# Performance work log

Hardware: AMD Instinct MI355X
Metric: run time of the kernel (lower is better)

## Reference

```python
import jax, jax.numpy as jnp
from jax import lax
import numpy as np

B, N, K = 8, 4096, 64          # clouds, points per cloud, max neighbors
N1, N2 = N // 2, N // 8        # fps ratio 0.5, then 0.25
R1, R2 = 0.2, 0.4              # ball-query radii


def setup_inputs() -> dict:
    key = jax.random.key(0)
    ks = jax.random.split(key, 7)
    def w(k, i, o):
        return jax.random.normal(k, (i, o), jnp.float32) / np.sqrt(i).astype(np.float32)
    return {
        "pos": jax.random.uniform(ks[0], (B, N, 3), jnp.float32),
        "w1a": w(ks[1], 3, 64),    "b1a": jnp.zeros(64, jnp.float32),
        "w1b": w(ks[2], 64, 64),   "b1b": jnp.zeros(64, jnp.float32),
        "w2a": w(ks[3], 67, 128),  "b2a": jnp.zeros(128, jnp.float32),
        "w2b": w(ks[4], 128, 128), "b2b": jnp.zeros(128, jnp.float32),
        "w3a": w(ks[5], 131, 256), "b3a": jnp.zeros(256, jnp.float32),
        "w3b": w(ks[6], 256, 1024),"b3b": jnp.zeros(1024, jnp.float32),
    }


def fps(pos, n_samples):
    # farthest point sampling, deterministic start at index 0. pos: [n, 3]
    d0 = jnp.sum((pos - pos[0]) ** 2, axis=-1)
    def step(mind, _):
        nxt = jnp.argmax(mind)
        d = jnp.sum((pos - pos[nxt]) ** 2, axis=-1)
        return jnp.minimum(mind, d), nxt
    _, idxs = lax.scan(step, d0, None, length=n_samples - 1)
    return jnp.concatenate([jnp.zeros((1,), idxs.dtype), idxs])


def ball_query(centers, pts, r):
    # up to K neighbors within radius r (nearest-first); centers are a subset of pts
    d2 = jnp.sum((centers[:, None, :] - pts[None, :, :]) ** 2, axis=-1)  # [M, n]
    neg = jnp.where(d2 <= r * r, -d2, -jnp.inf)
    vals, nbr = lax.top_k(neg, K)
    return nbr, vals > -jnp.inf  # [M, K] indices, validity mask


def mlp(x, w1, b1, w2, b2, relu_last):
    h = jax.nn.relu(x @ w1 + b1) @ w2 + b2
    return jax.nn.relu(h) if relu_last else h


def masked_max(h, mask):
    # max over neighbor axis; every center has itself as a valid neighbor
    return jnp.max(jnp.where(mask[..., None], h, -jnp.inf), axis=1)


def reference(pos, w1a, b1a, w1b, b1b, w2a, b2a, w2b, b2b, w3a, b3a, w3b, b3b):
    def single(p):  # p: [N, 3]
        # SA1: x is None -> per-edge input is relative position only
        idx1 = fps(p, N1)
        c1 = p[idx1]                                   # [N1, 3]
        nbr1, m1 = ball_query(c1, p, R1)               # [N1, K]
        rel1 = p[nbr1] - c1[:, None, :]                # [N1, K, 3]
        x1 = masked_max(mlp(rel1, w1a, b1a, w1b, b1b, True), m1)   # [N1, 64]
        # SA2: per-edge input is [x_j, pos_j - pos_i]
        idx2 = fps(c1, N2)
        c2 = c1[idx2]                                  # [N2, 3]
        nbr2, m2 = ball_query(c2, c1, R2)              # [N2, K]
        feat2 = jnp.concatenate([x1[nbr2], c1[nbr2] - c2[:, None, :]], axis=-1)  # [N2,K,67]
        x2 = masked_max(mlp(feat2, w2a, b2a, w2b, b2b, True), m2)  # [N2, 128]
        # Global SA: MLP on [x, pos] then global max pool
        g = mlp(jnp.concatenate([x2, c2], axis=-1), w3a, b3a, w3b, b3b, False)   # [N2,1024]
        return jnp.max(g, axis=0)                      # [1024]
    return jax.vmap(single)(pos)                       # [B, 1024]
```

## Files before the change

### kernel.cpp

```cpp
#include <hip/hip_runtime.h>
#include <cstdint>
#include <cstddef>


static constexpr int Bc = 8;
static constexpr int Np = 4096;
static constexpr int Kn = 64;
static constexpr int M1 = 2048;
static constexpr int M2 = 512;
static constexpr int LDX = 132;

#define DEVINL __device__ __forceinline__

DEVINL float d2_exact(float ax, float ay, float az, float bx, float by, float bz) {
    float dx = __fsub_rn(ax, bx);
    float dy = __fsub_rn(ay, by);
    float dz = __fsub_rn(az, bz);
    float xx = __fmul_rn(dx, dx);
    float yy = __fmul_rn(dy, dy);
    float zz = __fmul_rn(dz, dz);
    return __fadd_rn(__fadd_rn(xx, yy), zz);
}

template <int CTRL, int RM, int BM>
DEVINL unsigned long long dpp_max_step(unsigned long long k) {
    unsigned lo = (unsigned)k, hi = (unsigned)(k >> 32);
    unsigned slo = (unsigned)__builtin_amdgcn_update_dpp(0, (int)lo, CTRL, RM, BM, true);
    unsigned shi = (unsigned)__builtin_amdgcn_update_dpp(0, (int)hi, CTRL, RM, BM, true);
    unsigned long long s = ((unsigned long long)shi << 32) | (unsigned long long)slo;
    return s > k ? s : k;
}

DEVINL unsigned long long wave_max_u64_dpp(unsigned long long k) {
    k = dpp_max_step<0x111, 0xf, 0xf>(k);
    k = dpp_max_step<0x112, 0xf, 0xf>(k);
    k = dpp_max_step<0x114, 0xf, 0xf>(k);
    k = dpp_max_step<0x118, 0xf, 0xf>(k);
    k = dpp_max_step<0x142, 0xa, 0xf>(k);
    k = dpp_max_step<0x143, 0xc, 0xf>(k);
    return k;
}

DEVINL unsigned mort3(unsigned v) {
    return (v & 1u) | ((v & 2u) << 2) | ((v & 4u) << 4);
}

DEVINL unsigned cell_of(float x, float y, float z) {
    int ix = (int)(x * 8.0f); ix = ix < 0 ? 0 : (ix > 7 ? 7 : ix);
    int iy = (int)(y * 8.0f); iy = iy < 0 ? 0 : (iy > 7 ? 7 : iy);
    int iz = (int)(z * 8.0f); iz = iz < 0 ? 0 : (iz > 7 ? 7 : iz);
    return mort3((unsigned)ix) | (mort3((unsigned)iy) << 1) | (mort3((unsigned)iz) << 2);
}

DEVINL unsigned* scan512(unsigned* h0, unsigned* h1, int t) {
    unsigned* src = h0; unsigned* dst = h1;
    for (int d = 1; d < 512; d <<= 1) {
        unsigned v = src[t];
        if (t >= d) v += src[t - d];
        dst[t] = v;
        __syncthreads();
        unsigned* tmp = src; src = dst; dst = tmp;
    }
    return src;
}

template <int NPTS, int PT>
DEVINL void fps_chunk_body(const float* __restrict__ srcpts,
                           float4* __restrict__ scp_g,
                           float* __restrict__ mind_g,
                           char* smem, int t, int lane,
                           int s_begin, int s_end) {
    constexpr int NT = NPTS / PT;
    float4* scp = (float4*)smem;
    unsigned* h0 = (unsigned*)(smem + 65536);
    unsigned* h1 = (unsigned*)(smem + 67584);
    unsigned long long* slots = (unsigned long long*)(smem + 69632);
    float* journal = (float*)(smem + 69664);

    float px[PT], py[PT], pz[PT], mind[PT];
    unsigned oi[PT];
    unsigned long long ck = 0;

    if (s_begin == 0) {
        float gx[PT], gy[PT], gz[PT];
        unsigned gc[PT];
        #pragma unroll
        for (int j = 0; j < PT; ++j) {
            int p = j * NT + t;
            gx[j] = srcpts[p * 3 + 0];
            gy[j] = srcpts[p * 3 + 1];
            gz[j] = srcpts[p * 3 + 2];
            gc[j] = cell_of(gx[j], gy[j], gz[j]);
        }
        float x0 = srcpts[0], y0 = srcpts[1], z0 = srcpts[2];
        h0[t] = 0;
        if (t == 0) { slots[0] = 0; slots[1] = 0; slots[2] = 0; }
        __syncthreads();
        #pragma unroll
        for (int j = 0; j < PT; ++j) atomicAdd(&h0[gc[j]], 1u);
        __syncthreads();
        unsigned cnt = h0[t];
        unsigned* inc = scan512(h0, h1, t);
        inc[t] -= cnt;
        __syncthreads();
        #pragma unroll
        for (int j = 0; j < PT; ++j) {
            unsigned p = atomicAdd(&inc[gc[j]], 1u);
            unsigned key = ((0xFFFu - (unsigned)(j * NT + t)) << 12) | p;
            scp[p] = make_float4(gx[j], gy[j], gz[j], __uint_as_float(key));
        }
        __syncthreads();
        for (int k = t; k < NPTS; k += NT) scp_g[k] = scp[k];
        #pragma unroll
        for (int j = 0; j < PT; ++j) {
            float4 v = scp[t * PT + j];
            px[j] = v.x; py[j] = v.y; pz[j] = v.z;
            oi[j] = __float_as_uint(v.w);
        }
        #pragma unroll
        for (int j = 0; j < PT; ++j) {
            float d = d2_exact(px[j], py[j], pz[j], x0, y0, z0);
            mind[j] = d;
            unsigned long long kj =
                ((unsigned long long)__float_as_uint(d) << 24) | (unsigned long long)oi[j];
            if (kj > ck) ck = kj;
        }
        if (t == 0) { journal[0] = x0; journal[1] = y0; journal[2] = z0; }
    } else {
        if (t == 0) { slots[0] = 0; slots[1] = 0; slots[2] = 0; }
        for (int k = t; k < NPTS; k += NT) scp[k] = scp_g[k];
        __syncthreads();
        #pragma unroll
        for (int j = 0; j < PT; ++j) {
            float4 v = scp[t * PT + j];
            px[j] = v.x; py[j] = v.y; pz[j] = v.z;
            oi[j] = __float_as_uint(v.w);
        }
        #pragma unroll
        for (int j = 0; j < PT; ++j) mind[j] = mind_g[t * PT + j];
        #pragma unroll
        for (int j = 0; j < PT; ++j) {
            unsigned long long kj =
                ((unsigned long long)__float_as_uint(mind[j]) << 24) |
                (unsigned long long)oi[j];
            if (kj > ck) ck = kj;
        }
    }

    float lox = px[0], hix = px[0], loy = py[0], hiy = py[0], loz = pz[0], hiz = pz[0];
    #pragma unroll
    for (int j = 1; j < PT; ++j) {
        lox = fminf(lox, px[j]); hix = fmaxf(hix, px[j]);
        loy = fminf(loy, py[j]); hiy = fmaxf(hiy, py[j]);
        loz = fminf(loz, pz[j]); hiz = fmaxf(hiz, pz[j]);
    }

    float bmax = __uint_as_float((unsigned)(ck >> 24));
    unsigned long long wkey = wave_max_u64_dpp(ck);
    if (lane == 63) atomicMax(&slots[1], wkey);

    int rd = 1, wr = 2, rs = 0;
    for (int s = (s_begin == 0 ? 1 : s_begin); s < s_end; ++s) {
        __syncthreads();
        unsigned long long km = slots[rd];
        if (t == 0) slots[rs] = 0;
        unsigned spos = (unsigned)km & 0xFFFu;
        float4 cc = scp[spos];
        float cx = cc.x, cy = cc.y, cz = cc.z;
        if (t == 0) {
            int jj = (s - s_begin) * 3;
            journal[jj + 0] = cx; journal[jj + 1] = cy; journal[jj + 2] = cz;
        }
        float dxv = fmaxf(fmaxf(lox - cx, cx - hix), 0.0f);
        float dyv = fmaxf(fmaxf(loy - cy, cy - hiy), 0.0f);
        float dzv = fmaxf(fmaxf(loz - cz, cz - hiz), 0.0f);
        float L = dxv * dxv + dyv * dyv + dzv * dzv;
        bool fire = (L * 0.999f <= bmax);
        if (fire) {
            unsigned long long nck = 0;
            #pragma unroll
            for (int j = 0; j < PT; ++j) {
                float d = d2_exact(px[j], py[j], pz[j], cx, cy, cz);
                float m = fminf(mind[j], d);
                mind[j] = m;
                unsigned long long kj =
                    ((unsigned long long)__float_as_uint(m) << 24) | (unsigned long long)oi[j];
                if (kj > nck) nck = kj;
            }
            ck = nck;
            bmax = __uint_as_float((unsigned)(ck >> 24));
        }
        if (__ballot(fire) != 0ull) wkey = wave_max_u64_dpp(ck);
        if (lane == 63) atomicMax(&slots[wr], wkey);
        int nrd = wr; wr = rs; rs = rd; rd = nrd;
    }
    __syncthreads();
    #pragma unroll
    for (int j = 0; j < PT; ++j) mind_g[t * PT + j] = mind[j];
}

template <int NPT>
DEVINL void bq_core(const float* __restrict__ pb, float cx, float cy, float cz,
                    float r2, int* out, uint2* buf, int lane) {
    constexpr int CH = NPT / 64;
    constexpr int CAP = 1024;
    const unsigned r2b = __float_as_uint(r2);
    const unsigned long long lml = (1ull << lane) - 1ull;

    int cnt = 0;
    #pragma unroll 8
    for (int j = 0; j < CH; ++j) {
        int p = j * 64 + lane;
        float d = d2_exact(pb[p * 3 + 0], pb[p * 3 + 1], pb[p * 3 + 2], cx, cy, cz);
        cnt += __popcll(__ballot(__float_as_uint(d) <= r2b));
    }

    if (cnt <= Kn) {
        int basep = 0;
        #pragma unroll 8
        for (int j = 0; j < CH; ++j) {
            int p = j * 64 + lane;
            float d = d2_exact(pb[p * 3 + 0], pb[p * 3 + 1], pb[p * 3 + 2], cx, cy, cz);
            bool v = __float_as_uint(d) <= r2b;
            unsigned long long mk = __ballot(v);
            if (v) out[basep + __popcll(mk & lml)] = p;
            basep += __popcll(mk);
        }
        if (lane >= cnt) out[lane] = -1;
    } else if (cnt <= CAP) {
        int basep = 0;
        #pragma unroll 8
        for (int j = 0; j < CH; ++j) {
            int p = j * 64 + lane;
            float d = d2_exact(pb[p * 3 + 0], pb[p * 3 + 1], pb[p * 3 + 2], cx, cy, cz);
            unsigned ubj = __float_as_uint(d);
            bool v = ubj <= r2b;
            unsigned long long mk = __ballot(v);
            if (v) buf[basep + __popcll(mk & lml)] = make_uint2(ubj, (unsigned)p);
            basep += __popcll(mk);
        }
        const int C2 = (cnt + 63) >> 6;
        unsigned cb[CAP / 64], ci[CAP / 64];
        #pragma unroll
        for (int e = 0; e < CAP / 64; ++e) {
            if (e >= C2) break;
            int p = e * 64 + lane;
            uint2 v = buf[p];
            cb[e] = (p < cnt) ? v.x : 0xFFFFFFFFu;
            ci[e] = v.y;
        }
        unsigned lo = 0, hi = r2b;
        while (lo < hi) {
            unsigned mid = lo + ((hi - lo) >> 1);
            int c = 0;
            #pragma unroll
            for (int e = 0; e < CAP / 64; ++e) {
                if (e >= C2) break;
                c += __popcll(__ballot(cb[e] <= mid));
            }
            if (c >= Kn) hi = mid; else lo = mid + 1;
        }
        const unsigned tt = lo;
        int cntLess = 0;
        #pragma unroll
        for (int e = 0; e < CAP / 64; ++e) {
            if (e >= C2) break;
            cntLess += __popcll(__ballot(cb[e] < tt));
        }
        const int quota = Kn - cntLess;
        int baseLt = 0, eqseen = 0;
        #pragma unroll
        for (int e = 0; e < CAP / 64; ++e) {
            if (e >= C2) break;
            bool lt = cb[e] < tt;
            bool eq = cb[e] == tt;
            unsigned long long mlt = __ballot(lt);
            unsigned long long meq = __ballot(eq);
            if (lt) out[baseLt + __popcll(mlt & lml)] = (int)ci[e];
            if (eq) {
                int rr = eqseen + __popcll(meq & lml);
                if (rr < quota) out[cntLess + rr] = (int)ci[e];
            }
            baseLt += __popcll(mlt);
            eqseen += __popcll(meq);
        }
    } else {
        unsigned lo = 0, hi = r2b;
        while (lo < hi) {
            unsigned mid = lo + ((hi - lo) >> 1);
            int c = 0;
            for (int j = 0; j < CH; ++j) {
                int p = j * 64 + lane;
                float d = d2_exact(pb[p * 3 + 0], pb[p * 3 + 1], pb[p * 3 + 2], cx, cy, cz);
                c += __popcll(__ballot(__float_as_uint(d) <= mid));
            }
            if (c >= Kn) hi = mid; else lo = mid + 1;
        }
        const unsigned tt = lo;
        int cntLess = 0;
        for (int j = 0; j < CH; ++j) {
            int p = j * 64 + lane;
            float d = d2_exact(pb[p * 3 + 0], pb[p * 3 + 1], pb[p * 3 + 2], cx, cy, cz);
            cntLess += __popcll(__ballot(__float_as_uint(d) < tt));
        }
        const int quota = Kn - cntLess;
        int baseLt = 0, eqseen = 0;
        for (int j = 0; j < CH; ++j) {
            int p = j * 64 + lane;
            float d = d2_exact(pb[p * 3 + 0], pb[p * 3 + 1], pb[p * 3 + 2], cx, cy, cz);
            unsigned ubj = __float_as_uint(d);
            bool lt = ubj < tt;
            bool eq = ubj == tt;
            unsigned long long mlt = __ballot(lt);
            unsigned long long meq = __ballot(eq);
            if (lt) out[baseLt + __popcll(mlt & lml)] = p;
            if (eq) {
                int rr = eqseen + __popcll(meq & lml);
                if (rr < quota) out[cntLess + rr] = p;
            }
            baseLt += __popcll(mlt);
            eqseen += __popcll(meq);
        }
    }
}

DEVINL void mlp1_core(const float* __restrict__ pb, float cx, float cy, float cz,
                      const int* nbrL, const float* __restrict__ w1aT,
                      const float* __restrict__ w1bT, const float* __restrict__ b1b,
                      float* __restrict__ orow, int lane) {
    const int ii = nbrL[lane];
    const bool valid = ii >= 0;
    const int i2 = valid ? ii : 0;
    const float* pp = pb + (size_t)i2 * 3;
    float rx = pp[0] - cx, ry = pp[1] - cy, rz = pp[2] - cz;
    float h1[64];
    #pragma unroll
    for (int h = 0; h < 64; ++h) {
        float4 wv = ((const float4*)w1aT)[h];
        float a = fmaf(rx, wv.x, fmaf(ry, wv.y, fmaf(rz, wv.z, wv.w)));
        h1[h] = fmaxf(a, 0.0f);
    }
    for (int c4 = 0; c4 < 16; ++c4) {
        float v4[4];
        #pragma unroll
        for (int cq = 0; cq < 4; ++cq) {
            int c = c4 * 4 + cq;
            float acc = b1b[c];
            const float4* wr = (const float4*)(w1bT + (size_t)c * 64);
            #pragma unroll
            for (int q = 0; q < 16; ++q) {
                float4 wv = wr[q];
                acc = fmaf(h1[4 * q + 0], wv.x, acc);
                acc = fmaf(h1[4 * q + 1], wv.y, acc);
                acc = fmaf(h1[4 * q + 2], wv.z, acc);
                acc = fmaf(h1[4 * q + 3], wv.w, acc);
            }
            float v = fmaxf(acc, 0.0f);
            v = valid ? v : -__builtin_inff();
            #pragma unroll
            for (int o = 32; o > 0; o >>= 1) v = fmaxf(v, __shfl_xor(v, o, 64));
            v4[cq] = v;
        }
        if (lane == 0)
            ((float4*)orow)[c4] = make_float4(v4[0], v4[1], v4[2], v4[3]);
    }
}

DEVINL void mlp2_core(const float* __restrict__ x1b, const float* __restrict__ c1b,
                      float cx, float cy, float cz, const int* nbrL,
                      const float* __restrict__ w2aT, const float* __restrict__ w2bT,
                      const float* __restrict__ b2b, float* __restrict__ orow,
                      int lane) {
    const int ii = nbrL[lane];
    const bool valid = ii >= 0;
    const int i2 = valid ? ii : 0;

    float x[68];
    const float4* xr = (const float4*)(x1b + (size_t)i2 * 64);
    #pragma unroll
    for (int q = 0; q < 16; ++q) {
        float4 v = xr[q];
        x[4 * q + 0] = v.x; x[4 * q + 1] = v.y;
        x[4 * q + 2] = v.z; x[4 * q + 3] = v.w;
    }
    const float* cp = c1b + (size_t)i2 * 3;
    x[64] = cp[0] - cx;
    x[65] = cp[1] - cy;
    x[66] = cp[2] - cz;
    x[67] = 0.0f;

    float h1[128];
    #pragma unroll
    for (int h = 0; h < 128; ++h) {
        const float4* r4 = (const float4*)(w2aT + (size_t)h * 80);
        float acc = 0.0f;
        #pragma unroll
        for (int q = 0; q < 16; ++q) {
            float4 wv = r4[q];
            acc = fmaf(x[4 * q + 0], wv.x, acc);
            acc = fmaf(x[4 * q + 1], wv.y, acc);
            acc = fmaf(x[4 * q + 2], wv.z, acc);
            acc = fmaf(x[4 * q + 3], wv.w, acc);
        }
        float4 tl = r4[16];
        acc = fmaf(x[64], tl.x, acc);
        acc = fmaf(x[65], tl.y, acc);
        acc = fmaf(x[66], tl.z, acc);
        acc += tl.w;
        h1[h] = fmaxf(acc, 0.0f);
    }
    for (int c4 = 0; c4 < 32; ++c4) {
        float v4[4];
        #pragma unroll
        for (int cq = 0; cq < 4; ++cq) {
            int c = c4 * 4 + cq;
            float acc = b2b[c];
            const float4* wr = (const float4*)(w2bT + (size_t)c * 128);
            #pragma unroll
            for (int q = 0; q < 32; ++q) {
                float4 wv = wr[q];
                acc = fmaf(h1[4 * q + 0], wv.x, acc);
                acc = fmaf(h1[4 * q + 1], wv.y, acc);
                acc = fmaf(h1[4 * q + 2], wv.z, acc);
                acc = fmaf(h1[4 * q + 3], wv.w, acc);
            }
            float v = fmaxf(acc, 0.0f);
            v = valid ? v : -__builtin_inff();
            #pragma unroll
            for (int o = 32; o > 0; o >>= 1) v = fmaxf(v, __shfl_xor(v, o, 64));
            v4[cq] = v;
        }
        if (lane == 0) {
            orow[c4 * 4 + 0] = v4[0]; orow[c4 * 4 + 1] = v4[1];
            orow[c4 * 4 + 2] = v4[2]; orow[c4 * 4 + 3] = v4[3];
        }
    }
}

__global__ __launch_bounds__(512)
__attribute__((amdgpu_waves_per_eu(2, 2)))
void stage_kernel(int fps_stage, int s_begin, int s_end,
                  int w_stage, int w_begin, int wsh,
                  const float* __restrict__ pos, float* __restrict__ c1,
                  float* __restrict__ c2, float* __restrict__ X,
                  float* __restrict__ x1,
                  float4* __restrict__ scp1_g, float* __restrict__ mind1_g,
                  float4* __restrict__ scp2_g, float* __restrict__ mind2_g,
                  const float* __restrict__ w1a, const float* __restrict__ b1a,
                  const float* __restrict__ w1b, const float* __restrict__ w2a,
                  const float* __restrict__ b2a, const float* __restrict__ w2b,
                  float* __restrict__ w1aT, float* __restrict__ w1bT,
                  float* __restrict__ w2aT, float* __restrict__ w2bT,
                  const float* __restrict__ b1b, const float* __restrict__ b2b) {
    __shared__ __align__(16) char smem[94720];
    const int t = threadIdx.x;
    const int lane = t & 63;
    const int wid = t >> 6;

    if (fps_stage > 0 && blockIdx.x < Bc) {
        const int b = blockIdx.x;
        float* journal = (float*)(smem + 69664);
        if (fps_stage == 1) {
            fps_chunk_body<Np, 8>(pos + (size_t)b * Np * 3, scp1_g + (size_t)b * Np,
                                  mind1_g + (size_t)b * Np, smem, t, lane,
                                  s_begin, s_end);
            int n = (s_end - s_begin) * 3;
            for (int i = t; i < n; i += 512)
                c1[(size_t)b * M1 * 3 + s_begin * 3 + i] = journal[i];
        } else {
            fps_chunk_body<M1, 4>(c1 + (size_t)b * M1 * 3, scp2_g + (size_t)b * M1,
                                  mind2_g + (size_t)b * M1, smem, t, lane,
                                  s_begin, s_end);
            int n = (s_end - s_begin) * 3;
            for (int i = t; i < n; i += 512)
                c2[(size_t)b * M2 * 3 + s_begin * 3 + i] = journal[i];
            for (int i = t; i < n; i += 512) {
                int s = i / 3, k = i - s * 3;
                X[(size_t)(b * M2 + s_begin + s) * LDX + 128 + k] = journal[i];
            }
        }
        return;
    }

    const int wb = (fps_stage > 0) ? (int)blockIdx.x - Bc : (int)blockIdx.x;
    const int nw = (fps_stage > 0) ? (int)gridDim.x - Bc : (int)gridDim.x;

    if (w_stage == 1) {
        int i = wb * 512 + t;
        if (i < 64 * 4) {
            int h = i >> 2, d = i & 3;
            w1aT[i] = (d < 3) ? w1a[d * 64 + h] : b1a[h];
        }
        if (i < 64 * 64) {
            int c = i >> 6, h = i & 63;
            w1bT[i] = w1b[h * 64 + c];
        }
        if (i < 128 * 80) {
            int h = i / 80, d = i - h * 80;
            w2aT[i] = (d < 67) ? w2a[d * 128 + h] : ((d == 67) ? b2a[h] : 0.0f);
        }
        if (i < 128 * 128) {
            int c = i >> 7, h = i & 127;
            w2bT[i] = w2b[h * 128 + c];
        }
        return;
    }

    if (w_stage == 2) {
        uint2* cbuf = (uint2*)smem + (size_t)wid * 1024;
        int* nbrL = (int*)(smem + 65536) + wid * 64;
        const int span_mask = (1 << wsh) - 1;
        const int ntasks = Bc << wsh;
        for (int task = wb * 8 + wid; task < ntasks; task += nw * 8) {
            const int b = task >> wsh;
            const int s = w_begin + (task & span_mask);
            const int w = b * M1 + s;
            const float* cr = c1 + (size_t)w * 3;
            float cx = cr[0], cy = cr[1], cz = cr[2];
            const float* pb = pos + (size_t)b * Np * 3;
            bq_core<Np>(pb, cx, cy, cz, (float)(0.2 * 0.2), nbrL, cbuf, lane);
            mlp1_core(pb, cx, cy, cz, nbrL, w1aT, w1bT, b1b,
                      x1 + (size_t)w * 64, lane);
        }
        return;
    }

    if (w_stage == 3) {
        uint2* cbuf = (uint2*)smem + (size_t)wid * 1024;
        int* nbrL = (int*)(smem + 65536) + wid * 64;
        const int span_mask = (1 << wsh) - 1;
        const int ntasks = Bc << wsh;
        for (int task = wb * 8 + wid; task < ntasks; task += nw * 8) {
            const int b = task >> wsh;
            const int s = w_begin + (task & span_mask);
            const int w = b * M2 + s;
            const float* cr = c2 + (size_t)w * 3;
            float cx = cr[0], cy = cr[1], cz = cr[2];
            const float* c1b = c1 + (size_t)b * M1 * 3;
            bq_core<M1>(c1b, cx, cy, cz, (float)(0.4 * 0.4), nbrL, cbuf, lane);
            mlp2_core(x1 + (size_t)b * M1 * 64, c1b, cx, cy, cz, nbrL,
                      w2aT, w2bT, b2b, X + (size_t)w * LDX, lane);
        }
        return;
    }
}

__global__ __launch_bounds__(256)
void gemm1_kernel(const float* __restrict__ X, const float* __restrict__ w3a,
                  const float* __restrict__ b3a, float* __restrict__ H) {
    const int r = blockIdx.x;
    const int c = threadIdx.x;
    const float* xr = X + (size_t)r * LDX;
    float acc = b3a[c];
    for (int i = 0; i < 131; ++i)
        acc = fmaf(xr[i], w3a[(size_t)i * 256 + c], acc);
    H[(size_t)r * 256 + c] = fmaxf(acc, 0.0f);
}

__global__ __launch_bounds__(256)
void gemm2_kernel(const float* __restrict__ H, const float* __restrict__ w3b,
                  float* __restrict__ part) {
    __shared__ float As[32][33];
    __shared__ float Bs[32][64];
    __shared__ float red[8][64];
    const int bidx = blockIdx.x;
    const int nt = bidx & 15;
    const int mt = (bidx >> 4) & 15;
    const int b = bidx >> 8;
    const int row0 = b * M2 + mt * 32;
    const int col0 = nt * 64;
    const int t = threadIdx.x;
    const int rg = t >> 5, cg = t & 31;

    float acc[4][2] = {{0.f, 0.f}, {0.f, 0.f}, {0.f, 0.f}, {0.f, 0.f}};
    for (int k0 = 0; k0 < 256; k0 += 32) {
        #pragma unroll
        for (int q = 0; q < 4; ++q) {
            int id = t + q * 256;
            As[id >> 5][id & 31] = H[(size_t)(row0 + (id >> 5)) * 256 + k0 + (id & 31)];
        }
        #pragma unroll
        for (int q = 0; q < 8; ++q) {
            int id = t + q * 256;
            Bs[id >> 6][id & 63] = w3b[(size_t)(k0 + (id >> 6)) * 1024 + col0 + (id & 63)];
        }
        __syncthreads();
        #pragma unroll
        for (int kk = 0; kk < 32; ++kk) {
            float b0 = Bs[kk][cg * 2 + 0];
            float b1 = Bs[kk][cg * 2 + 1];
            #pragma unroll
            for (int j = 0; j < 4; ++j) {
                float a = As[rg * 4 + j][kk];
                acc[j][0] = fmaf(a, b0, acc[j][0]);
                acc[j][1] = fmaf(a, b1, acc[j][1]);
            }
        }
        __syncthreads();
    }
    float m0 = fmaxf(fmaxf(acc[0][0], acc[1][0]), fmaxf(acc[2][0], acc[3][0]));
    float m1 = fmaxf(fmaxf(acc[0][1], acc[1][1]), fmaxf(acc[2][1], acc[3][1]));
    red[rg][cg * 2 + 0] = m0;
    red[rg][cg * 2 + 1] = m1;
    __syncthreads();
    if (t < 64) {
        float v = red[0][t];
        #pragma unroll
        for (int q = 1; q < 8; ++q) v = fmaxf(v, red[q][t]);
        part[((size_t)b * 16 + mt) * 1024 + col0 + t] = v;
    }
}

__global__ __launch_bounds__(256)
void rmax_kernel(const float* __restrict__ part, const float* __restrict__ b3b,
                 float* __restrict__ out) {
    int i = blockIdx.x * 256 + threadIdx.x;
    int b = i >> 10, c = i & 1023;
    float v = -__builtin_inff();
    #pragma unroll
    for (int tt = 0; tt < 16; ++tt)
        v = fmaxf(v, part[((size_t)b * 16 + tt) * 1024 + c]);
    out[i] = v + b3b[c];
}

extern "C" void kernel_launch(void* const* d_in, const int* in_sizes, int n_in,
                              void* d_out, int out_size, void* d_ws, size_t ws_size,
                              hipStream_t stream) {
    const float* pos = (const float*)d_in[0];
    const float* w1a = (const float*)d_in[1];
    const float* b1a = (const float*)d_in[2];
    const float* w1b = (const float*)d_in[3];
    const float* b1b = (const float*)d_in[4];
    const float* w2a = (const float*)d_in[5];
    const float* b2a = (const float*)d_in[6];
    const float* w2b = (const float*)d_in[7];
    const float* b2b = (const float*)d_in[8];
    const float* w3a = (const float*)d_in[9];
    const float* b3a = (const float*)d_in[10];
    const float* w3b = (const float*)d_in[11];
    const float* b3b = (const float*)d_in[12];
    float* out = (float*)d_out;

    char* ws = (char*)d_ws;
    size_t off = 0;
    auto alloc = [&](size_t bytes) -> char* {
        char* p = ws + off;
        off += (bytes + 255) & ~(size_t)255;
        return p;
    };
    float*  c1     = (float*)alloc(sizeof(float) * Bc * M1 * 3);
    float*  c2     = (float*)alloc(sizeof(float) * Bc * M2 * 3);
    float*  x1     = (float*)alloc(sizeof(float) * Bc * M1 * 64);
    float*  X      = (float*)alloc(sizeof(float) * Bc * M2 * LDX);
    float*  H      = (float*)alloc(sizeof(float) * Bc * M2 * 256);
    float*  part   = (float*)alloc(sizeof(float) * Bc * 16 * 1024);
    float*  w1aT   = (float*)alloc(sizeof(float) * 64 * 4);
    float*  w1bT   = (float*)alloc(sizeof(float) * 64 * 64);
    float*  w2aT   = (float*)alloc(sizeof(float) * 128 * 80);
    float*  w2bT   = (float*)alloc(sizeof(float) * 128 * 128);
    float4* scp1_g = (float4*)alloc(sizeof(float4) * Bc * Np);
    float*  mind1g = (float*)alloc(sizeof(float) * Bc * Np);
    float4* scp2_g = (float4*)alloc(sizeof(float4) * Bc * M1);
    float*  mind2g = (float*)alloc(sizeof(float) * Bc * M1);

    auto launch = [&](int grid, int fs, int sb, int se, int wsg, int wbg, int wsh) {
        stage_kernel<<<dim3(grid), dim3(512), 0, stream>>>(
            fs, sb, se, wsg, wbg, wsh,
            pos, c1, c2, X, x1, scp1_g, mind1g, scp2_g, mind2g,
            w1a, b1a, w1b, w2a, b2a, w2b, w1aT, w1bT, w2aT, w2bT, b1b, b2b);
    };

    launch(Bc + 32, 1, 0, 512, 1, 0, 0);
    launch(Bc + 240, 1, 512, 1024, 2, 0, 9);
    launch(Bc + 240, 1, 1024, 1536, 2, 512, 9);
    launch(Bc + 240, 1, 1536, 2048, 2, 1024, 9);
    launch(Bc + 240, 2, 0, 256, 2, 1536, 9);
    launch(Bc + 240, 2, 256, 512, 3, 0, 8);
    launch(240, 0, 0, 0, 3, 256, 8);

    gemm1_kernel<<<dim3(Bc * M2), dim3(256), 0, stream>>>(X, w3a, b3a, H);
    gemm2_kernel<<<dim3(Bc * 16 * 16), dim3(256), 0, stream>>>(H, w3b, part);
    rmax_kernel<<<dim3(32), dim3(256), 0, stream>>>(part, b3b, out);
}
```

Before: 2.717 ms.

## Split neighbor MLPs out of stage kernel into standalone mlp1/mlp2 kernels

The stage kernel now only runs ball query and writes neighbor indices to new global buffers nbr1 and nbr2. Two new 256-thread kernels run the per-neighbor MLPs and max-pool after all FPS stages finish. This frees the MLP work from the stage kernel's heavy shared-memory footprint and its forced two-waves-per-EU limit, so it can run at higher occupancy. The cost is that the MLP work no longer overlaps with the serial FPS chain and now runs after it, plus an extra round trip of neighbor indices through global memory.

```diff
diff --git a/kernel.cpp b/kernel.cpp
--- a/kernel.cpp
+++ b/kernel.cpp
@@ -324,134 +324,20 @@
     }
 }
 
-DEVINL void mlp1_core(const float* __restrict__ pb, float cx, float cy, float cz,
-                      const int* nbrL, const float* __restrict__ w1aT,
-                      const float* __restrict__ w1bT, const float* __restrict__ b1b,
-                      float* __restrict__ orow, int lane) {
-    const int ii = nbrL[lane];
-    const bool valid = ii >= 0;
-    const int i2 = valid ? ii : 0;
-    const float* pp = pb + (size_t)i2 * 3;
-    float rx = pp[0] - cx, ry = pp[1] - cy, rz = pp[2] - cz;
-    float h1[64];
-    #pragma unroll
-    for (int h = 0; h < 64; ++h) {
-        float4 wv = ((const float4*)w1aT)[h];
-        float a = fmaf(rx, wv.x, fmaf(ry, wv.y, fmaf(rz, wv.z, wv.w)));
-        h1[h] = fmaxf(a, 0.0f);
-    }
-    for (int c4 = 0; c4 < 16; ++c4) {
-        float v4[4];
-        #pragma unroll
-        for (int cq = 0; cq < 4; ++cq) {
-            int c = c4 * 4 + cq;
-            float acc = b1b[c];
-            const float4* wr = (const float4*)(w1bT + (size_t)c * 64);
-            #pragma unroll
-            for (int q = 0; q < 16; ++q) {
-                float4 wv = wr[q];
-                acc = fmaf(h1[4 * q + 0], wv.x, acc);
-                acc = fmaf(h1[4 * q + 1], wv.y, acc);
-                acc = fmaf(h1[4 * q + 2], wv.z, acc);
-                acc = fmaf(h1[4 * q + 3], wv.w, acc);
-            }
-            float v = fmaxf(acc, 0.0f);
-            v = valid ? v : -__builtin_inff();
-            #pragma unroll
-            for (int o = 32; o > 0; o >>= 1) v = fmaxf(v, __shfl_xor(v, o, 64));
-            v4[cq] = v;
-        }
-        if (lane == 0)
-            ((float4*)orow)[c4] = make_float4(v4[0], v4[1], v4[2], v4[3]);
-    }
-}
-
-DEVINL void mlp2_core(const float* __restrict__ x1b, const float* __restrict__ c1b,
-                      float cx, float cy, float cz, const int* nbrL,
-                      const float* __restrict__ w2aT, const float* __restrict__ w2bT,
-                      const float* __restrict__ b2b, float* __restrict__ orow,
-                      int lane) {
-    const int ii = nbrL[lane];
-    const bool valid = ii >= 0;
-    const int i2 = valid ? ii : 0;
-
-    float x[68];
-    const float4* xr = (const float4*)(x1b + (size_t)i2 * 64);
-    #pragma unroll
-    for (int q = 0; q < 16; ++q) {
-        float4 v = xr[q];
-        x[4 * q + 0] = v.x; x[4 * q + 1] = v.y;
-        x[4 * q + 2] = v.z; x[4 * q + 3] = v.w;
-    }
-    const float* cp = c1b + (size_t)i2 * 3;
-    x[64] = cp[0] - cx;
-    x[65] = cp[1] - cy;
-    x[66] = cp[2] - cz;
-    x[67] = 0.0f;
-
-    float h1[128];
-    #pragma unroll
-    for (int h = 0; h < 128; ++h) {
-        const float4* r4 = (const float4*)(w2aT + (size_t)h * 80);
-        float acc = 0.0f;
-        #pragma unroll
-        for (int q = 0; q < 16; ++q) {
-            float4 wv = r4[q];
-            acc = fmaf(x[4 * q + 0], wv.x, acc);
-            acc = fmaf(x[4 * q + 1], wv.y, acc);
-            acc = fmaf(x[4 * q + 2], wv.z, acc);
-            acc = fmaf(x[4 * q + 3], wv.w, acc);
-        }
-        float4 tl = r4[16];
-        acc = fmaf(x[64], tl.x, acc);
-        acc = fmaf(x[65], tl.y, acc);
-        acc = fmaf(x[66], tl.z, acc);
-        acc += tl.w;
-        h1[h] = fmaxf(acc, 0.0f);
-    }
-    for (int c4 = 0; c4 < 32; ++c4) {
-        float v4[4];
-        #pragma unroll
-        for (int cq = 0; cq < 4; ++cq) {
-            int c = c4 * 4 + cq;
-            float acc = b2b[c];
-            const float4* wr = (const float4*)(w2bT + (size_t)c * 128);
-            #pragma unroll
-            for (int q = 0; q < 32; ++q) {
-                float4 wv = wr[q];
-                acc = fmaf(h1[4 * q + 0], wv.x, acc);
-                acc = fmaf(h1[4 * q + 1], wv.y, acc);
-                acc = fmaf(h1[4 * q + 2], wv.z, acc);
-                acc = fmaf(h1[4 * q + 3], wv.w, acc);
-            }
-            float v = fmaxf(acc, 0.0f);
-            v = valid ? v : -__builtin_inff();
-            #pragma unroll
-            for (int o = 32; o > 0; o >>= 1) v = fmaxf(v, __shfl_xor(v, o, 64));
-            v4[cq] = v;
-        }
-        if (lane == 0) {
-            orow[c4 * 4 + 0] = v4[0]; orow[c4 * 4 + 1] = v4[1];
-            orow[c4 * 4 + 2] = v4[2]; orow[c4 * 4 + 3] = v4[3];
-        }
-    }
-}
-
 __global__ __launch_bounds__(512)
 __attribute__((amdgpu_waves_per_eu(2, 2)))
 void stage_kernel(int fps_stage, int s_begin, int s_end,
                   int w_stage, int w_begin, int wsh,
                   const float* __restrict__ pos, float* __restrict__ c1,
                   float* __restrict__ c2, float* __restrict__ X,
-                  float* __restrict__ x1,
+                  int* __restrict__ nbr1, int* __restrict__ nbr2,
                   float4* __restrict__ scp1_g, float* __restrict__ mind1_g,
                   float4* __restrict__ scp2_g, float* __restrict__ mind2_g,
                   const float* __restrict__ w1a, const float* __restrict__ b1a,
                   const float* __restrict__ w1b, const float* __restrict__ w2a,
                   const float* __restrict__ b2a, const float* __restrict__ w2b,
                   float* __restrict__ w1aT, float* __restrict__ w1bT,
-                  float* __restrict__ w2aT, float* __restrict__ w2bT,
-                  const float* __restrict__ b1b, const float* __restrict__ b2b) {
+                  float* __restrict__ w2aT, float* __restrict__ w2bT) {
     __shared__ __align__(16) char smem[94720];
     const int t = threadIdx.x;
     const int lane = t & 63;
@@ -508,7 +394,6 @@
 
     if (w_stage == 2) {
         uint2* cbuf = (uint2*)smem + (size_t)wid * 1024;
-        int* nbrL = (int*)(smem + 65536) + wid * 64;
         const int span_mask = (1 << wsh) - 1;
         const int ntasks = Bc << wsh;
         for (int task = wb * 8 + wid; task < ntasks; task += nw * 8) {
@@ -516,18 +401,14 @@
             const int s = w_begin + (task & span_mask);
             const int w = b * M1 + s;
             const float* cr = c1 + (size_t)w * 3;
-            float cx = cr[0], cy = cr[1], cz = cr[2];
-            const float* pb = pos + (size_t)b * Np * 3;
-            bq_core<Np>(pb, cx, cy, cz, (float)(0.2 * 0.2), nbrL, cbuf, lane);
-            mlp1_core(pb, cx, cy, cz, nbrL, w1aT, w1bT, b1b,
-                      x1 + (size_t)w * 64, lane);
+            bq_core<Np>(pos + (size_t)b * Np * 3, cr[0], cr[1], cr[2],
+                        (float)(0.2 * 0.2), nbr1 + (size_t)w * Kn, cbuf, lane);
         }
         return;
     }
 
     if (w_stage == 3) {
         uint2* cbuf = (uint2*)smem + (size_t)wid * 1024;
-        int* nbrL = (int*)(smem + 65536) + wid * 64;
         const int span_mask = (1 << wsh) - 1;
         const int ntasks = Bc << wsh;
         for (int task = wb * 8 + wid; task < ntasks; task += nw * 8) {
@@ -535,13 +416,134 @@
             const int s = w_begin + (task & span_mask);
             const int w = b * M2 + s;
             const float* cr = c2 + (size_t)w * 3;
-            float cx = cr[0], cy = cr[1], cz = cr[2];
-            const float* c1b = c1 + (size_t)b * M1 * 3;
-            bq_core<M1>(c1b, cx, cy, cz, (float)(0.4 * 0.4), nbrL, cbuf, lane);
-            mlp2_core(x1 + (size_t)b * M1 * 64, c1b, cx, cy, cz, nbrL,
-                      w2aT, w2bT, b2b, X + (size_t)w * LDX, lane);
+            bq_core<M1>(c1 + (size_t)b * M1 * 3, cr[0], cr[1], cr[2],
+                        (float)(0.4 * 0.4), nbr2 + (size_t)w * Kn, cbuf, lane);
         }
         return;
+    }
+}
+
+__global__ __launch_bounds__(256)
+void mlp1_kernel(const float* __restrict__ pos, const float* __restrict__ c1,
+                 const int* __restrict__ nbr, const float* __restrict__ w1aT,
+                 const float* __restrict__ w1bT, const float* __restrict__ b1b,
+                 float* __restrict__ x1) {
+    const int lane = threadIdx.x & 63;
+    int w = __builtin_amdgcn_readfirstlane((int)(blockIdx.x * 4 + (threadIdx.x >> 6)));
+    const int b = w >> 11;
+    const int ii = nbr[(size_t)w * Kn + lane];
+    const bool valid = ii >= 0;
+    const int i2 = valid ? ii : 0;
+    const float* pp = pos + ((size_t)b * Np + i2) * 3;
+    const float* cc = c1 + (size_t)w * 3;
+    float rx = pp[0] - cc[0], ry = pp[1] - cc[1], rz = pp[2] - cc[2];
+    float h1[64];
+    #pragma unroll
+    for (int h = 0; h < 64; ++h) {
+        float4 wv = ((const float4*)w1aT)[h];
+        float a = fmaf(rx, wv.x, fmaf(ry, wv.y, fmaf(rz, wv.z, wv.w)));
+        h1[h] = fmaxf(a, 0.0f);
+    }
+    float* orow = x1 + (size_t)w * 64;
+    for (int c4 = 0; c4 < 16; ++c4) {
+        float v4[4];
+        #pragma unroll
+        for (int cq = 0; cq < 4; ++cq) {
+            int c = c4 * 4 + cq;
+            float acc = b1b[c];
+            const float4* wr = (const float4*)(w1bT + (size_t)c * 64);
+            #pragma unroll
+            for (int q = 0; q < 16; ++q) {
+                float4 wv = wr[q];
+                acc = fmaf(h1[4 * q + 0], wv.x, acc);
+                acc = fmaf(h1[4 * q + 1], wv.y, acc);
+                acc = fmaf(h1[4 * q + 2], wv.z, acc);
+                acc = fmaf(h1[4 * q + 3], wv.w, acc);
+            }
+            float v = fmaxf(acc, 0.0f);
+            v = valid ? v : -__builtin_inff();
+            #pragma unroll
+            for (int o = 32; o > 0; o >>= 1) v = fmaxf(v, __shfl_xor(v, o, 64));
+            v4[cq] = v;
+        }
+        if (lane == 0)
+            ((float4*)orow)[c4] = make_float4(v4[0], v4[1], v4[2], v4[3]);
+    }
+}
+
+__global__ __launch_bounds__(256)
+void mlp2_kernel(const float* __restrict__ x1, const float* __restrict__ c1,
+                 const float* __restrict__ c2, const int* __restrict__ nbr2,
+                 const float* __restrict__ w2aT, const float* __restrict__ w2bT,
+                 const float* __restrict__ b2b, float* __restrict__ X) {
+    const int lane = threadIdx.x & 63;
+    int w = __builtin_amdgcn_readfirstlane((int)(blockIdx.x * 4 + (threadIdx.x >> 6)));
+    const int b = w >> 9;
+    const int ii = nbr2[(size_t)w * Kn + lane];
+    const bool valid = ii >= 0;
+    const int i2 = valid ? ii : 0;
+
+    float x[68];
+    const float4* xr = (const float4*)(x1 + ((size_t)b * M1 + i2) * 64);
+    #pragma unroll
+    for (int q = 0; q < 16; ++q) {
+        float4 v = xr[q];
+        x[4 * q + 0] = v.x; x[4 * q + 1] = v.y;
+        x[4 * q + 2] = v.z; x[4 * q + 3] = v.w;
+    }
+    const float* cc = c2 + (size_t)w * 3;
+    const float* cp = c1 + ((size_t)b * M1 + i2) * 3;
+    x[64] = cp[0] - cc[0];
+    x[65] = cp[1] - cc[1];
+    x[66] = cp[2] - cc[2];
+    x[67] = 0.0f;
+
+    float h1[128];
+    #pragma unroll
+    for (int h = 0; h < 128; ++h) {
+        const float4* r4 = (const float4*)(w2aT + (size_t)h * 80);
+        float acc = 0.0f;
+        #pragma unroll
+        for (int q = 0; q < 16; ++q) {
+            float4 wv = r4[q];
+            acc = fmaf(x[4 * q + 0], wv.x, acc);
+            acc = fmaf(x[4 * q + 1], wv.y, acc);
+            acc = fmaf(x[4 * q + 2], wv.z, acc);
+            acc = fmaf(x[4 * q + 3], wv.w, acc);
+        }
+        float4 tl = r4[16];
+        acc = fmaf(x[64], tl.x, acc);
+        acc = fmaf(x[65], tl.y, acc);
+        acc = fmaf(x[66], tl.z, acc);
+        acc += tl.w;
+        h1[h] = fmaxf(acc, 0.0f);
+    }
+    float* orow = X + (size_t)w * LDX;
+    for (int c4 = 0; c4 < 32; ++c4) {
+        float v4[4];
+        #pragma unroll
+        for (int cq = 0; cq < 4; ++cq) {
+            int c = c4 * 4 + cq;
+            float acc = b2b[c];
+            const float4* wr = (const float4*)(w2bT + (size_t)c * 128);
+            #pragma unroll
+            for (int q = 0; q < 32; ++q) {
+                float4 wv = wr[q];
+                acc = fmaf(h1[4 * q + 0], wv.x, acc);
+                acc = fmaf(h1[4 * q + 1], wv.y, acc);
+                acc = fmaf(h1[4 * q + 2], wv.z, acc);
+                acc = fmaf(h1[4 * q + 3], wv.w, acc);
+            }
+            float v = fmaxf(acc, 0.0f);
+            v = valid ? v : -__builtin_inff();
+            #pragma unroll
+            for (int o = 32; o > 0; o >>= 1) v = fmaxf(v, __shfl_xor(v, o, 64));
+            v4[cq] = v;
+        }
+        if (lane == 0) {
+            orow[c4 * 4 + 0] = v4[0]; orow[c4 * 4 + 1] = v4[1];
+            orow[c4 * 4 + 2] = v4[2]; orow[c4 * 4 + 3] = v4[3];
+        }
     }
 }
 
@@ -650,6 +652,8 @@
     };
     float*  c1     = (float*)alloc(sizeof(float) * Bc * M1 * 3);
     float*  c2     = (float*)alloc(sizeof(float) * Bc * M2 * 3);
+    int*    nbr1   = (int*)alloc(sizeof(int) * Bc * M1 * Kn);
+    int*    nbr2   = (int*)alloc(sizeof(int) * Bc * M2 * Kn);
     float*  x1     = (float*)alloc(sizeof(float) * Bc * M1 * 64);
     float*  X      = (float*)alloc(sizeof(float) * Bc * M2 * LDX);
     float*  H      = (float*)alloc(sizeof(float) * Bc * M2 * 256);
@@ -666,8 +670,8 @@
     auto launch = [&](int grid, int fs, int sb, int se, int wsg, int wbg, int wsh) {
         stage_kernel<<<dim3(grid), dim3(512), 0, stream>>>(
             fs, sb, se, wsg, wbg, wsh,
-            pos, c1, c2, X, x1, scp1_g, mind1g, scp2_g, mind2g,
-            w1a, b1a, w1b, w2a, b2a, w2b, w1aT, w1bT, w2aT, w2bT, b1b, b2b);
+            pos, c1, c2, X, nbr1, nbr2, scp1_g, mind1g, scp2_g, mind2g,
+            w1a, b1a, w1b, w2a, b2a, w2b, w1aT, w1bT, w2aT, w2bT);
     };
 
     launch(Bc + 32, 1, 0, 512, 1, 0, 0);
@@ -678,6 +682,10 @@
     launch(Bc + 240, 2, 256, 512, 3, 0, 8);
     launch(240, 0, 0, 0, 3, 256, 8);
 
+    mlp1_kernel<<<dim3(Bc * M1 / 4), dim3(256), 0, stream>>>(
+        pos, c1, nbr1, w1aT, w1bT, b1b, x1);
+    mlp2_kernel<<<dim3(Bc * M2 / 4), dim3(256), 0, stream>>>(
+        x1, c1, c2, nbr2, w2aT, w2bT, b2b, X);
     gemm1_kernel<<<dim3(Bc * M2), dim3(256), 0, stream>>>(X, w3a, b3a, H);
     gemm2_kernel<<<dim3(Bc * 16 * 16), dim3(256), 0, stream>>>(H, w3b, part);
     rmax_kernel<<<dim3(32), dim3(256), 0, stream>>>(part, b3b, out);
```

Result: faster. 2.440 ms (-10.2%).
